# Optimization experiments

Measured on AMD Instinct MI355X. Metric: run time of the kernel, lower is better.

Reference implementation:

```python
import jax, jax.numpy as jnp
import numpy as np

D_MODEL = 1024
N_EXPERTS = 8
TOP_K = 2


def setup_inputs() -> dict:
    key = jax.random.key(0)
    ks = jax.random.split(key, 8)
    d, e = D_MODEL, N_EXPERTS
    s = 1.0 / np.sqrt(d)
    return {
        "x": jax.random.normal(ks[0], (4, 2048, d), dtype=jnp.float32),
        "W_gate": jax.random.uniform(ks[1], (d, e), jnp.float32, -s, s),
        "b_gate": jax.random.uniform(ks[2], (e,), jnp.float32, -s, s),
        "W1": jax.random.uniform(ks[3], (e, d, d), jnp.float32, -s, s),
        "b1": jax.random.uniform(ks[4], (e, d), jnp.float32, -s, s),
        "W2": jax.random.uniform(ks[5], (e, d, d), jnp.float32, -s, s),
        "b2": jax.random.uniform(ks[6], (e, d), jnp.float32, -s, s),
    }


def reference(x, W_gate, b_gate, W1, b1, W2, b2):
    B, T, d = x.shape
    xf = x.reshape(-1, d)  # [N, d], N = B*T
    # gating: raw linear scores, top-k selection; top-k raw scores are the
    # combine weights (original applies no softmax to gate scores)
    scores = xf @ W_gate + b_gate  # [N, E]
    topk_val, topk_idx = jax.lax.top_k(scores, TOP_K)  # [N, K]
    # scatter top-k weights into dense [N, E] combine matrix (indices distinct)
    onehot = jax.nn.one_hot(topk_idx, N_EXPERTS, dtype=xf.dtype)  # [N, K, E]
    w = jnp.einsum("nk,nke->ne", topk_val, onehot)  # [N, E]
    # run every expert MLP densely, then mask-combine (static shapes under jit)
    h = jax.nn.relu(jnp.einsum("nd,edh->neh", xf, W1) + b1)  # [N, E, d]
    y = jnp.einsum("neh,ehd->ned", h, W2) + b2  # [N, E, d]
    out = jnp.einsum("ned,ne->nd", y, w)  # weighted combine over experts
    return out.reshape(B, T, d)
```

## Files before the change

### kernel.cpp

```cpp
#include <hip/hip_runtime.h>
#include <hip/hip_bf16.h>


#define NTOK   8192
#define DM     1024
#define NE     8
#define BM     128
#define NSLOT  (NTOK * 2)
#define PADCAP (NSLOT + NE * BM)
#define MAXTILES (PADCAP / BM)

typedef __attribute__((ext_vector_type(8))) short  bf16x8;
typedef __attribute__((ext_vector_type(4))) float  f32x4;
typedef __attribute__((ext_vector_type(8))) unsigned short u16x8;

__device__ __forceinline__ unsigned short f2bf(float f) {
    union { float f; unsigned u; } v; v.f = f;
    unsigned r = v.u + 0x7fffu + ((v.u >> 16) & 1u);
    return (unsigned short)(r >> 16);
}

__device__ __forceinline__ void load_lds16(const ushort* g, ushort* l) {
    __builtin_amdgcn_global_load_lds(
        (const __attribute__((address_space(1))) unsigned int*)g,
        (__attribute__((address_space(3))) unsigned int*)l,
        16, 0, 0);
}

__global__ __launch_bounds__(256) void k_transpose2(const float* __restrict__ W1,
                                                    const float* __restrict__ W2,
                                                    ushort* __restrict__ w1t,
                                                    ushort* __restrict__ w2t,
                                                    int* __restrict__ counts) {
    int tid = threadIdx.x;
    if (blockIdx.x == 0 && blockIdx.y == 0 && blockIdx.z == 0 && tid < 16)
        counts[tid] = 0;
    int ez = blockIdx.z;
    const float* W = (ez < 8 ? W1 : W2) + (size_t)(ez & 7) * DM * DM;
    ushort* Wt = (ez < 8 ? w1t : w2t) + (size_t)(ez & 7) * DM * DM;
    __shared__ float t[64][65];
    int kt = blockIdx.y * 64, nt = blockIdx.x * 64;
    int r16 = tid >> 4, c4 = (tid & 15) * 4;
#pragma unroll
    for (int p = 0; p < 4; p++) {
        int k = p * 16 + r16;
        float4 v = *(const float4*)&W[(size_t)(kt + k) * DM + nt + c4];
        t[k][c4] = v.x; t[k][c4 + 1] = v.y; t[k][c4 + 2] = v.z; t[k][c4 + 3] = v.w;
    }
    __syncthreads();
    int n = tid >> 2, kb = (tid & 3) * 16;
#pragma unroll
    for (int h = 0; h < 2; h++) {
        int k0 = kb + h * 8;
        u16x8 o;
#pragma unroll
        for (int i = 0; i < 8; i++) o[i] = f2bf(t[k0 + i][n]);
        *(u16x8*)&Wt[(size_t)(nt + n) * DM + kt + k0] = o;
    }
}

__global__ __launch_bounds__(256) void k_gate(const float* __restrict__ x,
                                              const float* __restrict__ Wg,
                                              const float* __restrict__ bg,
                                              ushort* __restrict__ xb,
                                              int* __restrict__ tok_e,
                                              float* __restrict__ tok_w,
                                              int* __restrict__ counts,
                                              float* __restrict__ out,
                                              int* __restrict__ slot_token) {
    __shared__ float wgT[NE][DM];
    __shared__ int cnt[NE];
    int tid = threadIdx.x;
    if (tid < NE) cnt[tid] = 0;
    {
        float4 z4 = {0.f, 0.f, 0.f, 0.f};
        float4* orow = (float4*)(out + (size_t)blockIdx.x * 16 * DM);
#pragma unroll
        for (int i = 0; i < 16; i++) orow[i * 256 + tid] = z4;
        int s0 = blockIdx.x * 34;
        for (int i = tid; i < 34; i += 256) slot_token[s0 + i] = -1;
    }
    for (int i = tid; i < DM * NE; i += 256) {
        int d = i >> 3, e = i & 7;
        wgT[e][d] = Wg[i];
    }
    __syncthreads();
    int wave = tid >> 6, lane = tid & 63;
    int n0 = (blockIdx.x * 4 + wave) * 4;
    const float4* xr[4];
#pragma unroll
    for (int t = 0; t < 4; t++) xr[t] = (const float4*)(x + (size_t)(n0 + t) * DM);

    float acc[4][NE];
#pragma unroll
    for (int t = 0; t < 4; t++)
#pragma unroll
        for (int e = 0; e < NE; e++) acc[t][e] = 0.f;

#pragma unroll
    for (int j = 0; j < 4; j++) {
        float4 xv[4];
#pragma unroll
        for (int t = 0; t < 4; t++) xv[t] = xr[t][j * 64 + lane];
#pragma unroll
        for (int t = 0; t < 4; t++) {
            ushort4 o;
            o.x = f2bf(xv[t].x); o.y = f2bf(xv[t].y);
            o.z = f2bf(xv[t].z); o.w = f2bf(xv[t].w);
            ((ushort4*)xb)[(size_t)(n0 + t) * (DM / 4) + j * 64 + lane] = o;
        }
#pragma unroll
        for (int e = 0; e < NE; e++) {
            float4 wv = ((const float4*)&wgT[e][0])[j * 64 + lane];
#pragma unroll
            for (int t = 0; t < 4; t++) {
                acc[t][e] += xv[t].x * wv.x + xv[t].y * wv.y
                           + xv[t].z * wv.z + xv[t].w * wv.w;
            }
        }
    }
#pragma unroll
    for (int t = 0; t < 4; t++)
#pragma unroll
        for (int e = 0; e < NE; e++) {
#pragma unroll
            for (int off = 32; off >= 1; off >>= 1)
                acc[t][e] += __shfl_xor(acc[t][e], off);
        }
    if (lane < 4) {
        int t = lane, n = n0 + t;
        float sc[NE];
#pragma unroll
        for (int e = 0; e < NE; e++) sc[e] = acc[t][e] + bg[e];
        int e0 = 0; float v0 = sc[0];
#pragma unroll
        for (int e = 1; e < NE; e++) if (sc[e] > v0) { v0 = sc[e]; e0 = e; }
        int e1 = -1; float v1 = -3.0e38f;
#pragma unroll
        for (int e = 0; e < NE; e++) if (e != e0 && sc[e] > v1) { v1 = sc[e]; e1 = e; }
        tok_e[2 * n] = e0;     tok_w[2 * n] = v0;
        tok_e[2 * n + 1] = e1; tok_w[2 * n + 1] = v1;
        atomicAdd(&cnt[e0], 1);
        atomicAdd(&cnt[e1], 1);
    }
    __syncthreads();
    if (tid < NE) atomicAdd(&counts[tid], cnt[tid]);
}

__global__ __launch_bounds__(256) void k_fillplan(const int* __restrict__ tok_e,
                                                  const float* __restrict__ tok_w,
                                                  const int* __restrict__ counts,
                                                  int* __restrict__ cursor,
                                                  int* __restrict__ slot_token,
                                                  float* __restrict__ slot_w,
                                                  int* __restrict__ tile_e,
                                                  int* __restrict__ tile_b,
                                                  int* __restrict__ ntiles) {
    int tid = threadIdx.x;
    int cnts[NE];
#pragma unroll
    for (int e = 0; e < NE; e++) cnts[e] = counts[e];
    int base[NE]; int off = 0;
#pragma unroll
    for (int e = 0; e < NE; e++) {
        base[e] = off;
        off += ((cnts[e] + BM - 1) / BM) * BM;
    }
    if (blockIdx.x == 0 && tid == 0) {
        int t = 0, o2 = 0;
        for (int e = 0; e < NE; e++) {
            int nt = (cnts[e] + BM - 1) / BM;
            for (int i = 0; i < nt; i++) { tile_e[t] = e; tile_b[t] = o2 + i * BM; t++; }
            o2 += nt * BM;
        }
        *ntiles = t;
    }
    int n = blockIdx.x * 256 + tid;
#pragma unroll
    for (int k = 0; k < 2; k++) {
        int e = tok_e[2 * n + k];
        float w = tok_w[2 * n + k];
        int pos = atomicAdd(&cursor[e], 1);
        int s = base[e] + pos;
        slot_token[s] = n;
        slot_w[s] = w;
    }
}

template <int PHASE>
__global__ __launch_bounds__(256) void k_gemm(const ushort* __restrict__ A,
                                              const ushort* __restrict__ Wt,
                                              const float* __restrict__ bias,
                                              const int* __restrict__ slot_token,
                                              const float* __restrict__ slot_w,
                                              const int* __restrict__ tile_e,
                                              const int* __restrict__ tile_b,
                                              const int* __restrict__ ntiles,
                                              ushort* __restrict__ Hout,
                                              float* __restrict__ out) {
    int flat = blockIdx.x;
    int wid = (flat & 7) * MAXTILES + (flat >> 3);
    int t = wid >> 3;
    if (t >= *ntiles) return;
    int ncol0 = (wid & 7) << 7;
    int e = tile_e[t];
    int sbase = tile_b[t];

    __shared__ ushort As[2][8192];
    __shared__ ushort Bs[2][8192];

    int tid = threadIdx.x;
    int wave = tid >> 6, lane = tid & 63, quad = lane >> 4, lm = lane & 15;
    int wm = wave >> 1, wn = wave & 1;

    const ushort* Wte = Wt + (size_t)e * DM * DM;

    int sr = lane >> 3;
    int gseg = (lane & 7) ^ sr;
    const ushort* aptr[4];
    const ushort* bptr[4];
#pragma unroll
    for (int ci = 0; ci < 4; ci++) {
        int row = wave * 32 + ci * 8 + sr;
        int ar;
        if (PHASE == 1) {
            ar = slot_token[sbase + row];
            if (ar < 0) ar = 0;
        } else {
            ar = sbase + row;
        }
        aptr[ci] = A + (size_t)ar * DM + gseg * 8;
        bptr[ci] = Wte + (size_t)(ncol0 + row) * DM + gseg * 8;
    }

    f32x4 acc[4][4];
#pragma unroll
    for (int i = 0; i < 4; i++)
#pragma unroll
        for (int j = 0; j < 4; j++) acc[i][j] = (f32x4){0.f, 0.f, 0.f, 0.f};

    int asel = (quad ^ (lm & 7)) * 8;
    int abase = (wm * 64 + lm) * 64 + asel;
    int bbase = (wn * 64 + lm) * 64 + asel;

#define ISSUE(buf, koff)                                          \
    do {                                                          \
        _Pragma("unroll")                                         \
        for (int ci = 0; ci < 4; ci++)                            \
            load_lds16(aptr[ci] + (koff), &As[(buf)][(wave * 32 + ci * 8) * 64]); \
        _Pragma("unroll")                                         \
        for (int ci = 0; ci < 4; ci++)                            \
            load_lds16(bptr[ci] + (koff), &Bs[(buf)][(wave * 32 + ci * 8) * 64]); \
    } while (0)

#define COMPUTE(buf)                                                          \
    do {                                                                      \
        const ushort* Ab = As[(buf)];                                         \
        const ushort* Bb = Bs[(buf)];                                         \
        bf16x8 av0[4], bv0[4], av1[4], bv1[4];                                \
        _Pragma("unroll")                                                     \
        for (int f = 0; f < 4; f++) {                                         \
            av0[f] = *(const bf16x8*)&Ab[abase + f * 1024];                   \
            bv0[f] = *(const bf16x8*)&Bb[bbase + f * 1024];                   \
        }                                                                     \
        _Pragma("unroll")                                                     \
        for (int f = 0; f < 4; f++) {                                         \
            av1[f] = *(const bf16x8*)&Ab[(abase + f * 1024) ^ 32];            \
            bv1[f] = *(const bf16x8*)&Bb[(bbase + f * 1024) ^ 32];            \
        }                                                                     \
        __builtin_amdgcn_s_setprio(1);                                        \
        _Pragma("unroll")                                                     \
        for (int fm = 0; fm < 4; fm++)                                        \
            _Pragma("unroll")                                                 \
            for (int fn = 0; fn < 4; fn++)                                    \
                acc[fm][fn] = __builtin_amdgcn_mfma_f32_16x16x32_bf16(        \
                    av0[fm], bv0[fn], acc[fm][fn], 0, 0, 0);                  \
        _Pragma("unroll")                                                     \
        for (int fm = 0; fm < 4; fm++)                                        \
            _Pragma("unroll")                                                 \
            for (int fn = 0; fn < 4; fn++)                                    \
                acc[fm][fn] = __builtin_amdgcn_mfma_f32_16x16x32_bf16(        \
                    av1[fm], bv1[fn], acc[fm][fn], 0, 0, 0);                  \
        __builtin_amdgcn_s_setprio(0);                                        \
    } while (0)

    ISSUE(0, 0);
#pragma unroll 1
    for (int it = 0; it < 15; ++it) {
        ISSUE((it + 1) & 1, (it + 1) * 64);
        __builtin_amdgcn_s_waitcnt(0x0F78);
        __builtin_amdgcn_s_barrier();
        __builtin_amdgcn_sched_barrier(0);
        COMPUTE(it & 1);
        __builtin_amdgcn_sched_barrier(0);
        __builtin_amdgcn_s_waitcnt(0xC07F);
        __builtin_amdgcn_s_barrier();
    }
    __builtin_amdgcn_s_waitcnt(0x0F70);
    __builtin_amdgcn_s_barrier();
    __builtin_amdgcn_sched_barrier(0);
    COMPUTE(1);
#undef ISSUE
#undef COMPUTE

#pragma unroll
    for (int fm = 0; fm < 4; fm++) {
        int rowg = wm * 64 + fm * 16 + quad * 4;
        if (PHASE == 1) {
#pragma unroll
            for (int fn = 0; fn < 4; fn++) {
                int col = ncol0 + wn * 64 + fn * 16 + lm;
                float bv2 = bias[e * DM + col];
#pragma unroll
                for (int r = 0; r < 4; r++) {
                    float v = acc[fm][fn][r] + bv2;
                    v = fmaxf(v, 0.f);
                    Hout[(size_t)(sbase + rowg + r) * DM + col] = f2bf(v);
                }
            }
        } else {
            int tk[4]; float wv[4];
#pragma unroll
            for (int r = 0; r < 4; r++) {
                tk[r] = slot_token[sbase + rowg + r];
                wv[r] = slot_w[sbase + rowg + r];
            }
#pragma unroll
            for (int fn = 0; fn < 4; fn++) {
                int col = ncol0 + wn * 64 + fn * 16 + lm;
                float bv2 = bias[e * DM + col];
#pragma unroll
                for (int r = 0; r < 4; r++) {
                    if (tk[r] >= 0) {
                        float v = wv[r] * (acc[fm][fn][r] + bv2);
                        atomicAdd(&out[(size_t)tk[r] * DM + col], v);
                    }
                }
            }
        }
    }
}

extern "C" void kernel_launch(void* const* d_in, const int* in_sizes, int n_in,
                              void* d_out, int out_size, void* d_ws, size_t ws_size,
                              hipStream_t stream) {
    const float* x  = (const float*)d_in[0];
    const float* Wg = (const float*)d_in[1];
    const float* bg = (const float*)d_in[2];
    const float* W1 = (const float*)d_in[3];
    const float* b1 = (const float*)d_in[4];
    const float* W2 = (const float*)d_in[5];
    const float* b2 = (const float*)d_in[6];
    float* out = (float*)d_out;

    char* ws = (char*)d_ws;
    ushort* xb         = (ushort*)(ws + 0);
    ushort* w1t        = (ushort*)(ws + 16777216);
    ushort* w2t        = (ushort*)(ws + 33554432);
    ushort* H          = (ushort*)(ws + 50331648);
    int*    tok_e      = (int*)  (ws + 85983232);
    float*  tok_w      = (float*)(ws + 86048768);
    int*    slot_token = (int*)  (ws + 86114304);
    float*  slot_w     = (float*)(ws + 86183936);
    int*    counts     = (int*)  (ws + 86253568);
    int*    cursor     = counts + 8;
    int*    tile_e     = counts + 24;
    int*    tile_b     = tile_e + MAXTILES;
    int*    ntiles     = tile_b + MAXTILES;

    dim3 tg(16, 16, 16);
    k_transpose2<<<tg, 256, 0, stream>>>(W1, W2, w1t, w2t, counts);
    k_gate<<<NTOK / 16, 256, 0, stream>>>(x, Wg, bg, xb, tok_e, tok_w, counts,
                                          out, slot_token);
    k_fillplan<<<NTOK / 256, 256, 0, stream>>>(tok_e, tok_w, counts, cursor,
                                               slot_token, slot_w,
                                               tile_e, tile_b, ntiles);

    dim3 gg(8 * MAXTILES);
    k_gemm<1><<<gg, 256, 0, stream>>>(xb, w1t, b1, slot_token, slot_w,
                                      tile_e, tile_b, ntiles, H, nullptr);
    k_gemm<2><<<gg, 256, 0, stream>>>(H, w2t, b2, slot_token, slot_w,
                                      tile_e, tile_b, ntiles, nullptr, out);
}
```

Measured before the change: 404.0 us.

## Enlarge expert GEMM tiles to 256x256 with 8 waves and phased prefetch

Doubles the expert-GEMM block tile from 128x128 to 256x256 and uses 512 threads (8 waves, each computing 128x64), so each global load of A and B feeds twice as many MFMAs. The K-loop is restructured into sub-phases that interleave LDS fragment reads, staged prefetch of the next B tile, and MFMA bursts behind barriers. Slot padding per expert grows to BM=256, which adds wasted rows, and the workspace offsets and gate-side slot initialization are adjusted to match. The risks are more padding work, fewer blocks for occupancy, and higher register pressure from the 8x4 accumulator array.

```diff
diff --git a/kernel.cpp b/kernel.cpp
--- a/kernel.cpp
+++ b/kernel.cpp
@@ -5,7 +5,7 @@
 #define NTOK   8192
 #define DM     1024
 #define NE     8
-#define BM     128
+#define BM     256
 #define NSLOT  (NTOK * 2)
 #define PADCAP (NSLOT + NE * BM)
 #define MAXTILES (PADCAP / BM)
@@ -77,8 +77,8 @@
         float4* orow = (float4*)(out + (size_t)blockIdx.x * 16 * DM);
 #pragma unroll
         for (int i = 0; i < 16; i++) orow[i * 256 + tid] = z4;
-        int s0 = blockIdx.x * 34;
-        for (int i = tid; i < 34; i += 256) slot_token[s0 + i] = -1;
+        int s0 = blockIdx.x * (PADCAP / 512);
+        for (int i = tid; i < PADCAP / 512; i += 256) slot_token[s0 + i] = -1;
     }
     for (int i = tid; i < DM * NE; i += 256) {
         int d = i >> 3, e = i & 7;
@@ -188,7 +188,7 @@
 }
 
 template <int PHASE>
-__global__ __launch_bounds__(256) void k_gemm(const ushort* __restrict__ A,
+__global__ __launch_bounds__(512) void k_gemm(const ushort* __restrict__ A,
                                               const ushort* __restrict__ Wt,
                                               const float* __restrict__ bias,
                                               const int* __restrict__ slot_token,
@@ -199,19 +199,19 @@
                                               ushort* __restrict__ Hout,
                                               float* __restrict__ out) {
     int flat = blockIdx.x;
-    int wid = (flat & 7) * MAXTILES + (flat >> 3);
-    int t = wid >> 3;
+    int wid = (flat & 7) * (MAXTILES * 4 / 8) + (flat >> 3);
+    int t = wid >> 2;
     if (t >= *ntiles) return;
-    int ncol0 = (wid & 7) << 7;
+    int ncol0 = (wid & 3) << 8;
     int e = tile_e[t];
     int sbase = tile_b[t];
 
-    __shared__ ushort As[2][8192];
-    __shared__ ushort Bs[2][8192];
+    __shared__ ushort As[2][256 * 64];
+    __shared__ ushort Bs[2][256 * 64];
 
     int tid = threadIdx.x;
     int wave = tid >> 6, lane = tid & 63, quad = lane >> 4, lm = lane & 15;
-    int wm = wave >> 1, wn = wave & 1;
+    int wm = wave >> 2, wn = wave & 3;
 
     const ushort* Wte = Wt + (size_t)e * DM * DM;
 
@@ -219,93 +219,127 @@
     int gseg = (lane & 7) ^ sr;
     const ushort* aptr[4];
     const ushort* bptr[4];
-#pragma unroll
-    for (int ci = 0; ci < 4; ci++) {
-        int row = wave * 32 + ci * 8 + sr;
-        int ar;
-        if (PHASE == 1) {
-            ar = slot_token[sbase + row];
-            if (ar < 0) ar = 0;
-        } else {
-            ar = sbase + row;
-        }
-        aptr[ci] = A + (size_t)ar * DM + gseg * 8;
-        bptr[ci] = Wte + (size_t)(ncol0 + row) * DM + gseg * 8;
-    }
-
-    f32x4 acc[4][4];
-#pragma unroll
-    for (int i = 0; i < 4; i++)
+    int ldst[4];
+#pragma unroll
+    for (int h = 0; h < 2; h++)
+#pragma unroll
+        for (int ci = 0; ci < 2; ci++) {
+            int grow = h * 128 + wave * 16 + ci * 8 + sr;
+            int ar;
+            if (PHASE == 1) {
+                ar = slot_token[sbase + grow];
+                if (ar < 0) ar = 0;
+            } else {
+                ar = sbase + grow;
+            }
+            aptr[h * 2 + ci] = A + (size_t)ar * DM + gseg * 8;
+            bptr[h * 2 + ci] = Wte + (size_t)(ncol0 + grow) * DM + gseg * 8;
+            ldst[h * 2 + ci] = (h * 128 + wave * 16 + ci * 8) * 64;
+        }
+
+    f32x4 acc[8][4];
+#pragma unroll
+    for (int i = 0; i < 8; i++)
 #pragma unroll
         for (int j = 0; j < 4; j++) acc[i][j] = (f32x4){0.f, 0.f, 0.f, 0.f};
 
     int asel = (quad ^ (lm & 7)) * 8;
-    int abase = (wm * 64 + lm) * 64 + asel;
+    int abase = (wm * 128 + lm) * 64 + asel;
     int bbase = (wn * 64 + lm) * 64 + asel;
 
-#define ISSUE(buf, koff)                                          \
-    do {                                                          \
-        _Pragma("unroll")                                         \
-        for (int ci = 0; ci < 4; ci++)                            \
-            load_lds16(aptr[ci] + (koff), &As[(buf)][(wave * 32 + ci * 8) * 64]); \
-        _Pragma("unroll")                                         \
-        for (int ci = 0; ci < 4; ci++)                            \
-            load_lds16(bptr[ci] + (koff), &Bs[(buf)][(wave * 32 + ci * 8) * 64]); \
-    } while (0)
-
-#define COMPUTE(buf)                                                          \
-    do {                                                                      \
-        const ushort* Ab = As[(buf)];                                         \
-        const ushort* Bb = Bs[(buf)];                                         \
-        bf16x8 av0[4], bv0[4], av1[4], bv1[4];                                \
-        _Pragma("unroll")                                                     \
-        for (int f = 0; f < 4; f++) {                                         \
-            av0[f] = *(const bf16x8*)&Ab[abase + f * 1024];                   \
-            bv0[f] = *(const bf16x8*)&Bb[bbase + f * 1024];                   \
-        }                                                                     \
-        _Pragma("unroll")                                                     \
-        for (int f = 0; f < 4; f++) {                                         \
-            av1[f] = *(const bf16x8*)&Ab[(abase + f * 1024) ^ 32];            \
-            bv1[f] = *(const bf16x8*)&Bb[(bbase + f * 1024) ^ 32];            \
-        }                                                                     \
-        __builtin_amdgcn_s_setprio(1);                                        \
-        _Pragma("unroll")                                                     \
-        for (int fm = 0; fm < 4; fm++)                                        \
-            _Pragma("unroll")                                                 \
-            for (int fn = 0; fn < 4; fn++)                                    \
-                acc[fm][fn] = __builtin_amdgcn_mfma_f32_16x16x32_bf16(        \
-                    av0[fm], bv0[fn], acc[fm][fn], 0, 0, 0);                  \
-        _Pragma("unroll")                                                     \
-        for (int fm = 0; fm < 4; fm++)                                        \
-            _Pragma("unroll")                                                 \
-            for (int fn = 0; fn < 4; fn++)                                    \
-                acc[fm][fn] = __builtin_amdgcn_mfma_f32_16x16x32_bf16(        \
-                    av1[fm], bv1[fn], acc[fm][fn], 0, 0, 0);                  \
-        __builtin_amdgcn_s_setprio(0);                                        \
-    } while (0)
-
-    ISSUE(0, 0);
+    bf16x8 af[4][2], bf[4][2];
+
+#define STG_A(buf, h, koff) do { \
+        load_lds16(aptr[(h) * 2 + 0] + (koff), &As[(buf)][ldst[(h) * 2 + 0]]); \
+        load_lds16(aptr[(h) * 2 + 1] + (koff), &As[(buf)][ldst[(h) * 2 + 1]]); \
+    } while (0)
+#define STG_B(buf, h, koff) do { \
+        load_lds16(bptr[(h) * 2 + 0] + (koff), &Bs[(buf)][ldst[(h) * 2 + 0]]); \
+        load_lds16(bptr[(h) * 2 + 1] + (koff), &Bs[(buf)][ldst[(h) * 2 + 1]]); \
+    } while (0)
+#define LD_AF(Ab, fmb) do { \
+        _Pragma("unroll") \
+        for (int f = 0; f < 4; f++) { \
+            int o = abase + ((fmb) + f) * 1024; \
+            af[f][0] = *(const bf16x8*)&(Ab)[o]; \
+            af[f][1] = *(const bf16x8*)&(Ab)[o ^ 32]; \
+        } \
+    } while (0)
+#define LD_BF(Bb, fn) do { \
+        int o = bbase + (fn) * 1024; \
+        bf[fn][0] = *(const bf16x8*)&(Bb)[o]; \
+        bf[fn][1] = *(const bf16x8*)&(Bb)[o ^ 32]; \
+    } while (0)
+#define MM8(fmb, fn) do { \
+        _Pragma("unroll") \
+        for (int f = 0; f < 4; f++) { \
+            acc[(fmb) + f][(fn)] = __builtin_amdgcn_mfma_f32_16x16x32_bf16( \
+                af[f][0], bf[(fn)][0], acc[(fmb) + f][(fn)], 0, 0, 0); \
+            acc[(fmb) + f][(fn)] = __builtin_amdgcn_mfma_f32_16x16x32_bf16( \
+                af[f][1], bf[(fn)][1], acc[(fmb) + f][(fn)], 0, 0, 0); \
+        } \
+    } while (0)
+#define PH_SYNC() do { \
+        __builtin_amdgcn_s_barrier(); \
+        __builtin_amdgcn_s_waitcnt(0xC07F);  \
+        __builtin_amdgcn_sched_barrier(0); \
+    } while (0)
+#define PH_END() do { \
+        __builtin_amdgcn_sched_barrier(0); \
+        __builtin_amdgcn_s_barrier(); \
+    } while (0)
+#define KTILE(cur, nko, PF) do { \
+        const ushort* Ab = &As[(cur)][0]; \
+        const ushort* Bb = &Bs[(cur)][0]; \
+         \
+        LD_AF(Ab, 0); LD_BF(Bb, 0); LD_BF(Bb, 1); \
+        if (PF) STG_B((cur) ^ 1, 0, (nko)); \
+        PH_SYNC(); \
+        __builtin_amdgcn_s_setprio(1); MM8(0, 0); MM8(0, 1); __builtin_amdgcn_s_setprio(0); \
+        PH_END(); \
+         \
+        LD_BF(Bb, 2); LD_BF(Bb, 3); \
+        if (PF) STG_B((cur) ^ 1, 1, (nko)); \
+        PH_SYNC(); \
+        __builtin_amdgcn_s_setprio(1); MM8(0, 2); MM8(0, 3); __builtin_amdgcn_s_setprio(0); \
+        PH_END(); \
+         \
+        LD_AF(Ab, 4); \
+        PH_SYNC(); \
+        __builtin_amdgcn_s_setprio(1); MM8(4, 0); MM8(4, 1); __builtin_amdgcn_s_setprio(0); \
+        PH_END(); \
+         \
+        __builtin_amdgcn_s_setprio(1); MM8(4, 2); MM8(4, 3); __builtin_amdgcn_s_setprio(0); \
+        __builtin_amdgcn_sched_barrier(0); \
+    } while (0)
+
+    STG_A(0, 0, 0); STG_A(0, 1, 0); STG_B(0, 0, 0); STG_B(0, 1, 0);
 #pragma unroll 1
-    for (int it = 0; it < 15; ++it) {
-        ISSUE((it + 1) & 1, (it + 1) * 64);
-        __builtin_amdgcn_s_waitcnt(0x0F78);
+    for (int kt = 0; kt < 15; ++kt) {
+        int cur = kt & 1;
+        int nko = (kt + 1) * 64;
+        STG_A(cur ^ 1, 0, nko); STG_A(cur ^ 1, 1, nko);
+        __builtin_amdgcn_s_waitcnt(0x0F74);
         __builtin_amdgcn_s_barrier();
         __builtin_amdgcn_sched_barrier(0);
-        COMPUTE(it & 1);
-        __builtin_amdgcn_sched_barrier(0);
-        __builtin_amdgcn_s_waitcnt(0xC07F);
-        __builtin_amdgcn_s_barrier();
+        KTILE(cur, nko, 1);
     }
     __builtin_amdgcn_s_waitcnt(0x0F70);
     __builtin_amdgcn_s_barrier();
     __builtin_amdgcn_sched_barrier(0);
-    COMPUTE(1);
-#undef ISSUE
-#undef COMPUTE
-
-#pragma unroll
-    for (int fm = 0; fm < 4; fm++) {
-        int rowg = wm * 64 + fm * 16 + quad * 4;
+    KTILE(1, 0, 0);
+#undef STG_A
+#undef STG_B
+#undef LD_AF
+#undef LD_BF
+#undef MM8
+#undef PH_SYNC
+#undef PH_END
+#undef KTILE
+
+#pragma unroll
+    for (int fm = 0; fm < 8; fm++) {
+        int rowg = wm * 128 + fm * 16 + quad * 4;
         if (PHASE == 1) {
 #pragma unroll
             for (int fn = 0; fn < 4; fn++) {
@@ -358,11 +392,11 @@
     ushort* w1t        = (ushort*)(ws + 16777216);
     ushort* w2t        = (ushort*)(ws + 33554432);
     ushort* H          = (ushort*)(ws + 50331648);
-    int*    tok_e      = (int*)  (ws + 85983232);
-    float*  tok_w      = (float*)(ws + 86048768);
-    int*    slot_token = (int*)  (ws + 86114304);
-    float*  slot_w     = (float*)(ws + 86183936);
-    int*    counts     = (int*)  (ws + 86253568);
+    int*    tok_e      = (int*)  (ws + 88080384);
+    float*  tok_w      = (float*)(ws + 88145920);
+    int*    slot_token = (int*)  (ws + 88211456);
+    float*  slot_w     = (float*)(ws + 88285184);
+    int*    counts     = (int*)  (ws + 88358912);
     int*    cursor     = counts + 8;
     int*    tile_e     = counts + 24;
     int*    tile_b     = tile_e + MAXTILES;
@@ -376,9 +410,9 @@
                                                slot_token, slot_w,
                                                tile_e, tile_b, ntiles);
 
-    dim3 gg(8 * MAXTILES);
-    k_gemm<1><<<gg, 256, 0, stream>>>(xb, w1t, b1, slot_token, slot_w,
+    dim3 gg(4 * MAXTILES);
+    k_gemm<1><<<gg, 512, 0, stream>>>(xb, w1t, b1, slot_token, slot_w,
                                       tile_e, tile_b, ntiles, H, nullptr);
-    k_gemm<2><<<gg, 256, 0, stream>>>(H, w2t, b2, slot_token, slot_w,
+    k_gemm<2><<<gg, 512, 0, stream>>>(H, w2t, b2, slot_token, slot_w,
                                       tile_e, tile_b, ntiles, nullptr, out);
 }
```

After: 439.2 us. +8.7%, slower.
